# Kernel optimization log

Hardware: AMD Instinct MI355X
Metric: run time of the kernel (lower is better)

The kernel has to match this reference:

```python
import jax, jax.numpy as jnp
import numpy as np

N = 50000       # nodes
E = 500000      # edges (before self loops)
IN = 256        # in_dim
HID = 128       # hidden
HEADS = 2       # GATv2 heads (concat=False -> head mean)
G = 64          # num graphs in batch
SLOPE = 0.2     # leaky_relu negative slope (PyG default)


def setup_inputs() -> dict:
    key = jax.random.key(0)
    ks = jax.random.split(key, 30)
    w = lambda k, shape: jax.random.normal(k, shape, jnp.float32) * 0.05
    inp = {
        "x": jax.random.normal(ks[0], (N, IN), jnp.float32),
        "edge_index": jax.random.randint(ks[1], (2, E), 0, N, dtype=jnp.int64),
        "batch": jnp.sort(jax.random.randint(ks[2], (N,), 0, G, dtype=jnp.int64)),
        # encoder MLP
        "enc_w1": w(ks[3], (HID, IN)),  "enc_b1": w(ks[4], (HID,)),
        "enc_w2": w(ks[5], (HID, HID)), "enc_b2": w(ks[6], (HID,)),
        # GATv2 conv1: lin_l, lin_r -> heads*out; att [H, C]; final bias [C]
        "c1_wl": w(ks[7], (HEADS * HID, HID)),  "c1_bl": w(ks[8], (HEADS * HID,)),
        "c1_wr": w(ks[9], (HEADS * HID, HID)),  "c1_br": w(ks[10], (HEADS * HID,)),
        "c1_att": w(ks[11], (HEADS, HID)),       "c1_bias": w(ks[12], (HID,)),
        # GATv2 conv2
        "c2_wl": w(ks[13], (HEADS * HID, HID)), "c2_bl": w(ks[14], (HEADS * HID,)),
        "c2_wr": w(ks[15], (HEADS * HID, HID)), "c2_br": w(ks[16], (HEADS * HID,)),
        "c2_att": w(ks[17], (HEADS, HID)),       "c2_bias": w(ks[18], (HID,)),
        # attentional pooling gate MLP
        "gate_w1": w(ks[19], (HID, HID)), "gate_b1": w(ks[20], (HID,)),
        "gate_w2": w(ks[21], (1, HID)),   "gate_b2": w(ks[22], (1,)),
        # head MLP
        "head_w1": w(ks[23], (HID, HID)), "head_b1": w(ks[24], (HID,)),
        "head_w2": w(ks[25], (2, HID)),   "head_b2": w(ks[26], (2,)),
    }
    return inp


def _gatv2(x, src, dst, wl, bl, wr, br, att, bias):
    """PyG GATv2Conv, heads=HEADS, concat=False (mean over heads)."""
    n = x.shape[0]
    xl = (x @ wl.T + bl).reshape(n, HEADS, HID)   # source transform
    xr = (x @ wr.T + br).reshape(n, HEADS, HID)   # target transform
    s = jax.nn.leaky_relu(xl[src] + xr[dst], SLOPE)          # [E,H,C]
    e = jnp.einsum('ehc,hc->eh', s, att)                      # [E,H]
    m = jax.ops.segment_max(e, dst, num_segments=n)
    a = jnp.exp(e - m[dst])
    a = a / (jax.ops.segment_sum(a, dst, num_segments=n)[dst] + 1e-16)
    out = jax.ops.segment_sum(a[:, :, None] * xl[src], dst, num_segments=n)
    return out.mean(axis=1) + bias                            # [N,C]


def _forward(x, edge_index, batch,
             enc_w1, enc_b1, enc_w2, enc_b2,
             c1_wl, c1_bl, c1_wr, c1_br, c1_att, c1_bias,
             c2_wl, c2_bl, c2_wr, c2_br, c2_att, c2_bias,
             gate_w1, gate_b1, gate_w2, gate_b2,
             head_w1, head_b1, head_w2, head_b2):
    n = x.shape[0]
    # add self loops (PyG GATv2Conv default add_self_loops=True)
    loop = jnp.arange(n, dtype=edge_index.dtype)
    src = jnp.concatenate([edge_index[0], loop])
    dst = jnp.concatenate([edge_index[1], loop])

    h = jax.nn.relu(x @ enc_w1.T + enc_b1)
    h = jax.nn.relu(h @ enc_w2.T + enc_b2)
    h = jax.nn.relu(_gatv2(h, src, dst, c1_wl, c1_bl, c1_wr, c1_br, c1_att, c1_bias))
    h = jax.nn.relu(_gatv2(h, src, dst, c2_wl, c2_bl, c2_wr, c2_br, c2_att, c2_bias))

    # attentional aggregation: segment-softmax gate over graphs
    gate = (jax.nn.relu(h @ gate_w1.T + gate_b1) @ gate_w2.T + gate_b2)[:, 0]  # [N]
    gm = jax.ops.segment_max(gate, batch, num_segments=G)
    ga = jnp.exp(gate - gm[batch])
    ga = ga / (jax.ops.segment_sum(ga, batch, num_segments=G)[batch] + 1e-16)
    g = jax.ops.segment_sum(ga[:, None] * h, batch, num_segments=G)  # [G,HID]

    out = jax.nn.relu(g @ head_w1.T + head_b1) @ head_w2.T + head_b2  # [G,2]
    # F.normalize(dim=1), eps=1e-12
    norm = jnp.linalg.norm(out, axis=1, keepdims=True)
    return out / jnp.maximum(norm, 1e-12)


def reference(x, edge_index, batch,
              enc_w1, enc_b1, enc_w2, enc_b2,
              c1_wl, c1_bl, c1_wr, c1_br, c1_att, c1_bias,
              c2_wl, c2_bl, c2_wr, c2_br, c2_att, c2_bias,
              gate_w1, gate_b1, gate_w2, gate_b2,
              head_w1, head_b1, head_w2, head_b2):
    return _forward(x, edge_index, batch,
                    enc_w1, enc_b1, enc_w2, enc_b2,
                    c1_wl, c1_bl, c1_wr, c1_br, c1_att, c1_bias,
                    c2_wl, c2_bl, c2_wr, c2_br, c2_att, c2_bias,
                    gate_w1, gate_b1, gate_w2, gate_b2,
                    head_w1, head_b1, head_w2, head_b2)
```

## Files before the change

### kernel.cpp

```cpp
#include <hip/hip_runtime.h>
#include <math.h>

#define CH 128
#define F2 256
#define NG 64
#define PS 16

typedef __attribute__((ext_vector_type(8))) short short8;
typedef __attribute__((ext_vector_type(4))) float f32x4;

__device__ inline ushort f2bf_t(float x) { return (ushort)(__float_as_uint(x) >> 16); }
__device__ inline ushort f2bf_r(float x) {
  uint u = __float_as_uint(x);
  return (ushort)((u + 0x7fffu + ((u >> 16) & 1u)) >> 16);
}
__device__ inline float bf2f(ushort h) { return __uint_as_float(((uint)h) << 16); }

__device__ inline void split4(const float4 v, ushort4& h, ushort4& l) {
  h.x = f2bf_t(v.x); l.x = f2bf_t(v.x - bf2f(h.x));
  h.y = f2bf_t(v.y); l.y = f2bf_t(v.y - bf2f(h.y));
  h.z = f2bf_t(v.z); l.z = f2bf_t(v.z - bf2f(h.z));
  h.w = f2bf_t(v.w); l.w = f2bf_t(v.w - bf2f(h.w));
}

template<int NT, int ACT, int AF32, int GATE>
__global__ __launch_bounds__(NT * 128) void gemm_full(
    const void* __restrict__ Av, const float* __restrict__ W,
    const float* __restrict__ bias, ushort* __restrict__ Cb,
    const float* __restrict__ w2, const float* __restrict__ b2,
    float* __restrict__ gate, int M, int K) {
  constexpr int Nn = NT * 64;
  constexpr int NTH = NT * 128;
  constexpr int AC4 = AF32 ? (1024 / NTH) : 1;
  constexpr int AC2 = AF32 ? 1 : (512 / NTH);
  __shared__ ushort Ab[128 * 40];
  __shared__ ushort Wh[Nn * 40], Wl[Nn * 40];
  const int tid = threadIdx.x;
  const int lane = tid & 63, wid = tid >> 6;
  const int wm = wid / NT, wn = wid % NT;
  const int bm = blockIdx.x * 128;
  const int fr = lane & 15, fg = lane >> 4;
  const float* Af = (const float*)Av;
  const ushort* Ah16 = (const ushort*)Av;

  f32x4 acc[4][4];
#pragma unroll
  for (int i = 0; i < 4; ++i)
#pragma unroll
    for (int j = 0; j < 4; ++j) acc[i][j] = (f32x4)0.f;

  float4 avf[AC4];
  short8 avb[AC2];
  float4 wv[4];
  auto load_tiles = [&](int k0) {
    if constexpr (AF32) {
#pragma unroll
      for (int i2 = 0; i2 < AC4; ++i2) {
        const int c = tid + NTH * i2;
        const int row = c >> 3, kq = (c & 7) * 4;
        const int gr = bm + row;
        avf[i2] = (gr < M) ? *(const float4*)(Af + (size_t)gr * K + k0 + kq)
                           : make_float4(0.f, 0.f, 0.f, 0.f);
      }
    } else {
#pragma unroll
      for (int i2 = 0; i2 < AC2; ++i2) {
        const int c = tid + NTH * i2;
        const int row = c >> 2, kq = (c & 3) * 8;
        const int gr = bm + row;
        avb[i2] = (gr < M) ? *(const short8*)(Ah16 + (size_t)gr * K + k0 + kq)
                           : (short8)0;
      }
    }
#pragma unroll
    for (int i2 = 0; i2 < 4; ++i2) {
      const int c = tid + NTH * i2;
      const int row = c >> 3, kq = (c & 7) * 4;
      wv[i2] = *(const float4*)(W + (size_t)row * K + k0 + kq);
    }
  };

  load_tiles(0);
  for (int k0 = 0; k0 < K; k0 += 32) {
    __syncthreads();
    if constexpr (AF32) {
#pragma unroll
      for (int i2 = 0; i2 < AC4; ++i2) {
        const int c = tid + NTH * i2;
        const int row = c >> 3, kq = (c & 7) * 4;
        const float4 v = avf[i2];
        ushort4 h;
        h.x = f2bf_r(v.x); h.y = f2bf_r(v.y); h.z = f2bf_r(v.z); h.w = f2bf_r(v.w);
        *(ushort4*)&Ab[row * 40 + kq] = h;
      }
    } else {
#pragma unroll
      for (int i2 = 0; i2 < AC2; ++i2) {
        const int c = tid + NTH * i2;
        const int row = c >> 2, kq = (c & 3) * 8;
        *(short8*)&Ab[row * 40 + kq] = avb[i2];
      }
    }
#pragma unroll
    for (int i2 = 0; i2 < 4; ++i2) {
      const int c = tid + NTH * i2;
      const int row = c >> 3, kq = (c & 7) * 4;
      ushort4 h, l; split4(wv[i2], h, l);
      *(ushort4*)&Wh[row * 40 + kq] = h;
      *(ushort4*)&Wl[row * 40 + kq] = l;
    }
    __syncthreads();
    if (k0 + 32 < K) load_tiles(k0 + 32);
    short8 fa[4];
#pragma unroll
    for (int i = 0; i < 4; ++i)
      fa[i] = *(const short8*)&Ab[(wm * 64 + i * 16 + fr) * 40 + fg * 8];
#pragma unroll
    for (int j = 0; j < 4; ++j) {
      const int wbase = (wn * 64 + j * 16 + fr) * 40 + fg * 8;
      const short8 fwh = *(const short8*)&Wh[wbase];
      const short8 fwl = *(const short8*)&Wl[wbase];
#pragma unroll
      for (int i = 0; i < 4; ++i) {
        acc[i][j] = __builtin_amdgcn_mfma_f32_16x16x32_bf16(fa[i], fwh, acc[i][j], 0, 0, 0);
        acc[i][j] = __builtin_amdgcn_mfma_f32_16x16x32_bf16(fa[i], fwl, acc[i][j], 0, 0, 0);
      }
    }
  }
  if constexpr (GATE) {
    __shared__ float gpart[2][128];
    const float b2v = b2[0];
    float rsum[4][4];
#pragma unroll
    for (int i = 0; i < 4; ++i)
#pragma unroll
      for (int r = 0; r < 4; ++r) rsum[i][r] = 0.f;
#pragma unroll
    for (int j = 0; j < 4; ++j) {
      const int col = wn * 64 + j * 16 + fr;
      const float bv = bias[col], wv2 = w2[col];
#pragma unroll
      for (int i = 0; i < 4; ++i)
#pragma unroll
        for (int r = 0; r < 4; ++r) {
          const float v = fmaxf(acc[i][j][r] + bv, 0.f);
          rsum[i][r] += v * wv2;
        }
    }
#pragma unroll
    for (int i = 0; i < 4; ++i)
#pragma unroll
      for (int r = 0; r < 4; ++r) {
        float v = rsum[i][r];
        v += __shfl_xor(v, 1);
        v += __shfl_xor(v, 2);
        v += __shfl_xor(v, 4);
        v += __shfl_xor(v, 8);
        rsum[i][r] = v;
      }
    if (fr == 0) {
#pragma unroll
      for (int i = 0; i < 4; ++i)
#pragma unroll
        for (int r = 0; r < 4; ++r)
          gpart[wn][wm * 64 + i * 16 + fg * 4 + r] = rsum[i][r];
    }
    __syncthreads();
    if (tid < 128) {
      const int row = bm + tid;
      if (row < M) gate[row] = gpart[0][tid] + gpart[1][tid] + b2v;
    }
  } else {
#pragma unroll
    for (int j = 0; j < 4; ++j) {
      const int col = wn * 64 + j * 16 + fr;
      const float bv = bias[col];
#pragma unroll
      for (int i = 0; i < 4; ++i)
#pragma unroll
        for (int r = 0; r < 4; ++r) {
          const int row = bm + wm * 64 + i * 16 + fg * 4 + r;
          if (row < M) {
            float v = acc[i][j][r] + bv;
            if (ACT) v = fmaxf(v, 0.f);
            Cb[(size_t)row * Nn + col] = f2bf_r(v);
          }
        }
    }
  }
}

__global__ void fill_zero_i32(int* __restrict__ p, int n) {
  int i = blockIdx.x * blockDim.x + threadIdx.x;
  if (i < n) p[i] = 0;
}
__global__ void edge_hist(const int* __restrict__ ei, int E, int Etot, int* __restrict__ counts) {
  int e = blockIdx.x * blockDim.x + threadIdx.x;
  if (e >= Etot) return;
  int d = (e < E) ? ei[E + e] : (e - E);
  atomicAdd(&counts[d], 1);
}
__global__ __launch_bounds__(1024) void hist_sums(const int* __restrict__ counts,
                                                  int* __restrict__ bsum, int n) {
  __shared__ int sm[1024];
  const int tid = threadIdx.x;
  const int idx = blockIdx.x * 1024 + tid;
  sm[tid] = (idx < n) ? counts[idx] : 0;
  __syncthreads();
  for (int off = 512; off; off >>= 1) {
    if (tid < off) sm[tid] += sm[tid + off];
    __syncthreads();
  }
  if (tid == 0) bsum[blockIdx.x] = sm[0];
}
__global__ void scan_bsums(const int* __restrict__ bsum, int* __restrict__ boff, int nb) {
  if (threadIdx.x == 0 && blockIdx.x == 0) {
    int run = 0;
    for (int i = 0; i < nb; ++i) { boff[i] = run; run += bsum[i]; }
  }
}
__global__ __launch_bounds__(1024) void scan_apply(const int* __restrict__ counts,
                                                   const int* __restrict__ boff,
                                                   int* __restrict__ indptr,
                                                   int* __restrict__ cur, int n) {
  __shared__ int sm[1024];
  const int tid = threadIdx.x;
  const int idx = blockIdx.x * 1024 + tid;
  const int v = (idx < n) ? counts[idx] : 0;
  sm[tid] = v;
  __syncthreads();
  for (int off = 1; off < 1024; off <<= 1) {
    const int t = (tid >= off) ? sm[tid - off] : 0;
    __syncthreads();
    sm[tid] += t;
    __syncthreads();
  }
  const int excl = boff[blockIdx.x] + sm[tid] - v;
  if (idx < n) {
    indptr[idx] = excl;
    cur[idx] = excl;
    if (idx == n - 1) indptr[n] = excl + v;
  }
}
__global__ void edge_scatter(const int* __restrict__ ei, int E, int Etot,
                             int* __restrict__ cur, int* __restrict__ csr_src) {
  int e = blockIdx.x * blockDim.x + threadIdx.x;
  if (e >= Etot) return;
  int s, d;
  if (e < E) { s = ei[e]; d = ei[E + e]; } else { s = e - E; d = s; }
  int p = atomicAdd(&cur[d], 1);
  csr_src[p] = s;
}

__global__ __launch_bounds__(256) void fused_conv(
    const int* __restrict__ indptr, const int* __restrict__ csr_src,
    const ushort* __restrict__ XLb, const ushort* __restrict__ XRb,
    const float* __restrict__ att, const float* __restrict__ bias,
    ushort* __restrict__ OUT, int N) {
  int node = (int)((blockIdx.x * (size_t)256 + threadIdx.x) >> 6);
  if (node >= N) return;
  const int lane = threadIdx.x & 63;
  const int f = lane * 4;
  const ushort4 xrb = *(const ushort4*)(XRb + (size_t)node * F2 + f);
  const float xr0 = bf2f(xrb.x), xr1 = bf2f(xrb.y), xr2 = bf2f(xrb.z), xr3 = bf2f(xrb.w);
  const float4 at = *(const float4*)(att + f);
  const int s = indptr[node], e = indptr[node + 1];
  float m = -3.4e38f, dsum = 0.f;
  float a0 = 0.f, a1 = 0.f, a2 = 0.f, a3 = 0.f;

  auto score = [&](float x0, float x1, float x2, float x3) -> float {
    float v0 = x0 + xr0; v0 = v0 > 0.f ? v0 : 0.2f * v0;
    float v1 = x1 + xr1; v1 = v1 > 0.f ? v1 : 0.2f * v1;
    float v2 = x2 + xr2; v2 = v2 > 0.f ? v2 : 0.2f * v2;
    float v3 = x3 + xr3; v3 = v3 > 0.f ? v3 : 0.2f * v3;
    return v0 * at.x + v1 * at.y + v2 * at.z + v3 * at.w;
  };
  auto update = [&](float p, float x0, float x1, float x2, float x3) {
    if (__all(p <= m)) {
      const float w = __expf(p - m);
      dsum += w;
      a0 += w * x0; a1 += w * x1; a2 += w * x2; a3 += w * x3;
    } else {
      const float mn = fmaxf(m, p);
      const float sc = __expf(m - mn);
      const float w  = __expf(p - mn);
      dsum = dsum * sc + w;
      a0 = a0 * sc + w * x0; a1 = a1 * sc + w * x1;
      a2 = a2 * sc + w * x2; a3 = a3 * sc + w * x3;
      m = mn;
    }
  };

  int k = s;
  for (; k + 4 <= e; k += 4) {
    const int sn0 = csr_src[k + 0];
    const int sn1 = csr_src[k + 1];
    const int sn2 = csr_src[k + 2];
    const int sn3 = csr_src[k + 3];
    const ushort4 b0 = *(const ushort4*)(XLb + (size_t)sn0 * F2 + f);
    const ushort4 b1 = *(const ushort4*)(XLb + (size_t)sn1 * F2 + f);
    const ushort4 b2 = *(const ushort4*)(XLb + (size_t)sn2 * F2 + f);
    const ushort4 b3 = *(const ushort4*)(XLb + (size_t)sn3 * F2 + f);
    const float x00 = bf2f(b0.x), x01 = bf2f(b0.y), x02 = bf2f(b0.z), x03 = bf2f(b0.w);
    const float x10 = bf2f(b1.x), x11 = bf2f(b1.y), x12 = bf2f(b1.z), x13 = bf2f(b1.w);
    const float x20 = bf2f(b2.x), x21 = bf2f(b2.y), x22 = bf2f(b2.z), x23 = bf2f(b2.w);
    const float x30 = bf2f(b3.x), x31 = bf2f(b3.y), x32 = bf2f(b3.z), x33 = bf2f(b3.w);
    float p0 = score(x00, x01, x02, x03);
    float p1 = score(x10, x11, x12, x13);
    float p2 = score(x20, x21, x22, x23);
    float p3 = score(x30, x31, x32, x33);
#pragma unroll
    for (int d2 = 1; d2 <= 16; d2 <<= 1) {
      p0 += __shfl_xor(p0, d2);
      p1 += __shfl_xor(p1, d2);
      p2 += __shfl_xor(p2, d2);
      p3 += __shfl_xor(p3, d2);
    }
    update(p0, x00, x01, x02, x03);
    update(p1, x10, x11, x12, x13);
    update(p2, x20, x21, x22, x23);
    update(p3, x30, x31, x32, x33);
  }
  for (; k < e; ++k) {
    const int sn = csr_src[k];
    const ushort4 xb = *(const ushort4*)(XLb + (size_t)sn * F2 + f);
    const float x0 = bf2f(xb.x), x1 = bf2f(xb.y), x2 = bf2f(xb.z), x3 = bf2f(xb.w);
    float p = score(x0, x1, x2, x3);
#pragma unroll
    for (int d2 = 1; d2 <= 16; d2 <<= 1) p += __shfl_xor(p, d2);
    update(p, x0, x1, x2, x3);
  }

  const float inv = 1.f / (dsum + 1e-16f);
  a0 *= inv; a1 *= inv; a2 *= inv; a3 *= inv;
  float o0 = 0.5f * (a0 + __shfl_xor(a0, 32));
  float o1 = 0.5f * (a1 + __shfl_xor(a1, 32));
  float o2 = 0.5f * (a2 + __shfl_xor(a2, 32));
  float o3 = 0.5f * (a3 + __shfl_xor(a3, 32));
  if (lane < 32) {
    ushort4 r;
    r.x = f2bf_r(fmaxf(o0 + bias[f + 0], 0.f));
    r.y = f2bf_r(fmaxf(o1 + bias[f + 1], 0.f));
    r.z = f2bf_r(fmaxf(o2 + bias[f + 2], 0.f));
    r.w = f2bf_r(fmaxf(o3 + bias[f + 3], 0.f));
    *(ushort4*)(OUT + (size_t)node * CH + f) = r;
  }
}

__global__ __launch_bounds__(256) void pool_stats(
    const float* __restrict__ gate, const int* __restrict__ batch,
    float* __restrict__ pm, float* __restrict__ pd, int N) {
  const int g = blockIdx.x, tid = threadIdx.x;
  int lo = 0, hi = N;
  while (lo < hi) { int mid = (lo + hi) >> 1; if (batch[mid] < g) lo = mid + 1; else hi = mid; }
  const int s = lo;
  lo = 0; hi = N;
  while (lo < hi) { int mid = (lo + hi) >> 1; if (batch[mid] < g + 1) lo = mid + 1; else hi = mid; }
  const int e = lo;
  __shared__ float red[256];
  float m = -3.4e38f;
  for (int n = s + tid; n < e; n += 256) m = fmaxf(m, gate[n]);
  red[tid] = m; __syncthreads();
  for (int off = 128; off; off >>= 1) {
    if (tid < off) red[tid] = fmaxf(red[tid], red[tid + off]);
    __syncthreads();
  }
  m = red[0]; __syncthreads();
  float d = 0.f;
  for (int n = s + tid; n < e; n += 256) d += expf(gate[n] - m);
  red[tid] = d; __syncthreads();
  for (int off = 128; off; off >>= 1) {
    if (tid < off) red[tid] += red[tid + off];
    __syncthreads();
  }
  if (tid == 0) { pm[g] = m; pd[g] = red[0]; }
}

__global__ __launch_bounds__(128) void pool_partial(
    const float* __restrict__ gate, const int* __restrict__ batch,
    const float* __restrict__ pm, const float* __restrict__ pd,
    const ushort* __restrict__ H, float* __restrict__ PART, int N) {
  const int g = blockIdx.x / PS, j = blockIdx.x % PS;
  const int tid = threadIdx.x;
  int lo = 0, hi = N;
  while (lo < hi) { int mid = (lo + hi) >> 1; if (batch[mid] < g) lo = mid + 1; else hi = mid; }
  const int s = lo;
  lo = 0; hi = N;
  while (lo < hi) { int mid = (lo + hi) >> 1; if (batch[mid] < g + 1) lo = mid + 1; else hi = mid; }
  const int e = lo;
  const int len = e - s;
  const int per = (len + PS - 1) / PS;
  const int ns = s + j * per;
  const int ne = min(ns + per, e);
  const float m = pm[g];
  const float inv = 1.f / (pd[g] + 1e-16f);
  float acc = 0.f;
  for (int n = ns; n < ne; ++n) {
    const float w = expf(gate[n] - m);
    acc += w * bf2f(H[(size_t)n * CH + tid]);
  }
  PART[(size_t)blockIdx.x * CH + tid] = acc * inv;
}
__global__ __launch_bounds__(128) void pool_reduce(
    const float* __restrict__ PART, float* __restrict__ Gout) {
  const int g = blockIdx.x, tid = threadIdx.x;
  float acc = 0.f;
#pragma unroll
  for (int j = 0; j < PS; ++j) acc += PART[(size_t)(g * PS + j) * CH + tid];
  Gout[(size_t)g * CH + tid] = acc;
}

__global__ __launch_bounds__(128) void head_kernel(
    const float* __restrict__ Gin, const float* __restrict__ w1, const float* __restrict__ b1,
    const float* __restrict__ w2, const float* __restrict__ b2, float* __restrict__ out) {
  const int g = blockIdx.x, tid = threadIdx.x;
  __shared__ float gs[128], ts[128], o[2];
  gs[tid] = Gin[(size_t)g * CH + tid];
  __syncthreads();
  float a = b1[tid];
  for (int k = 0; k < CH; ++k) a += w1[tid * CH + k] * gs[k];
  ts[tid] = fmaxf(a, 0.f);
  __syncthreads();
  if (tid < 2) {
    float v = b2[tid];
    for (int d2 = 0; d2 < CH; ++d2) v += w2[tid * CH + d2] * ts[d2];
    o[tid] = v;
  }
  __syncthreads();
  if (tid == 0) {
    float nrm = sqrtf(o[0] * o[0] + o[1] * o[1]);
    nrm = fmaxf(nrm, 1e-12f);
    out[g * 2 + 0] = o[0] / nrm;
    out[g * 2 + 1] = o[1] / nrm;
  }
}

extern "C" void kernel_launch(void* const* d_in, const int* in_sizes, int n_in,
                              void* d_out, int out_size, void* d_ws, size_t ws_size,
                              hipStream_t stream) {
  const float* x       = (const float*)d_in[0];
  const int*   ei      = (const int*)d_in[1];
  const int*   batch   = (const int*)d_in[2];
  const float* enc_w1  = (const float*)d_in[3];
  const float* enc_b1  = (const float*)d_in[4];
  const float* enc_w2  = (const float*)d_in[5];
  const float* enc_b2  = (const float*)d_in[6];
  const float* c1_wl   = (const float*)d_in[7];
  const float* c1_bl   = (const float*)d_in[8];
  const float* c1_wr   = (const float*)d_in[9];
  const float* c1_br   = (const float*)d_in[10];
  const float* c1_att  = (const float*)d_in[11];
  const float* c1_bias = (const float*)d_in[12];
  const float* c2_wl   = (const float*)d_in[13];
  const float* c2_bl   = (const float*)d_in[14];
  const float* c2_wr   = (const float*)d_in[15];
  const float* c2_br   = (const float*)d_in[16];
  const float* c2_att  = (const float*)d_in[17];
  const float* c2_bias = (const float*)d_in[18];
  const float* gate_w1 = (const float*)d_in[19];
  const float* gate_b1 = (const float*)d_in[20];
  const float* gate_w2 = (const float*)d_in[21];
  const float* gate_b2 = (const float*)d_in[22];
  const float* head_w1 = (const float*)d_in[23];
  const float* head_b1 = (const float*)d_in[24];
  const float* head_w2 = (const float*)d_in[25];
  const float* head_b2 = (const float*)d_in[26];

  const int N    = in_sizes[2];
  const int E    = in_sizes[1] / 2;
  const int INF_ = in_sizes[0] / N;
  const int Etot = E + N;
  const int NBLK = (N + 1023) / 1024;

  char* wp = (char*)d_ws;
  auto alloc = [&](size_t bytes) -> void* {
    void* p = (void*)wp;
    wp += (bytes + 255) & ~(size_t)255;
    return p;
  };
  ushort* XLb    = (ushort*)alloc((size_t)N * F2 * 2);
  ushort* XRb    = (ushort*)alloc((size_t)N * F2 * 2);
  ushort* Ha     = (ushort*)alloc((size_t)N * CH * 2);
  ushort* Hb     = (ushort*)alloc((size_t)N * CH * 2);
  ushort* Hc     = (ushort*)alloc((size_t)N * CH * 2);
  int*    counts = (int*)alloc((size_t)N * 4);
  int*    indptr = (int*)alloc((size_t)(N + 1) * 4);
  int*    cur    = (int*)alloc((size_t)N * 4);
  int*    csr_src= (int*)alloc((size_t)Etot * 4);
  int*    bsum   = (int*)alloc((size_t)NBLK * 4);
  int*    boff   = (int*)alloc((size_t)NBLK * 4);
  float*  gateb  = (float*)alloc((size_t)N * 4);
  float*  GS     = (float*)alloc((size_t)NG * CH * 4);
  float*  pm     = (float*)alloc((size_t)NG * 4);
  float*  pd     = (float*)alloc((size_t)NG * 4);
  float*  PART   = (float*)alloc((size_t)NG * PS * CH * 4);

  const dim3 blk(256);
  const int gM = (N + 127) / 128;

  gemm_full<2,1,1,0><<<gM, 256, 0, stream>>>(x, enc_w1, enc_b1, Ha,
                                             nullptr, nullptr, nullptr, N, INF_);
  gemm_full<2,1,0,0><<<gM, 256, 0, stream>>>(Ha, enc_w2, enc_b2, Hb,
                                             nullptr, nullptr, nullptr, N, CH);

  fill_zero_i32<<<(N + 255) / 256, blk, 0, stream>>>(counts, N);
  edge_hist<<<(Etot + 255) / 256, blk, 0, stream>>>(ei, E, Etot, counts);
  hist_sums<<<NBLK, 1024, 0, stream>>>(counts, bsum, N);
  scan_bsums<<<1, 64, 0, stream>>>(bsum, boff, NBLK);
  scan_apply<<<NBLK, 1024, 0, stream>>>(counts, boff, indptr, cur, N);
  edge_scatter<<<(Etot + 255) / 256, blk, 0, stream>>>(ei, E, Etot, cur, csr_src);

  gemm_full<4,0,0,0><<<gM, 512, 0, stream>>>(Hb, c1_wl, c1_bl, XLb,
                                             nullptr, nullptr, nullptr, N, CH);
  gemm_full<4,0,0,0><<<gM, 512, 0, stream>>>(Hb, c1_wr, c1_br, XRb,
                                             nullptr, nullptr, nullptr, N, CH);
  fused_conv<<<(N + 3) / 4, blk, 0, stream>>>(indptr, csr_src, XLb, XRb, c1_att, c1_bias, Hc, N);

  gemm_full<4,0,0,0><<<gM, 512, 0, stream>>>(Hc, c2_wl, c2_bl, XLb,
                                             nullptr, nullptr, nullptr, N, CH);
  gemm_full<4,0,0,0><<<gM, 512, 0, stream>>>(Hc, c2_wr, c2_br, XRb,
                                             nullptr, nullptr, nullptr, N, CH);
  fused_conv<<<(N + 3) / 4, blk, 0, stream>>>(indptr, csr_src, XLb, XRb, c2_att, c2_bias, Hb, N);

  gemm_full<2,1,0,1><<<gM, 256, 0, stream>>>(Hb, gate_w1, gate_b1, nullptr,
                                             gate_w2, gate_b2, gateb, N, CH);

  pool_stats<<<NG, blk, 0, stream>>>(gateb, batch, pm, pd, N);
  pool_partial<<<NG * PS, 128, 0, stream>>>(gateb, batch, pm, pd, Hb, PART, N);
  pool_reduce<<<NG, 128, 0, stream>>>(PART, GS);

  head_kernel<<<NG, 128, 0, stream>>>(GS, head_w1, head_b1, head_w2, head_b2, (float*)d_out);
}
```

Before: 535.2 us.

## Pre-split weights to bf16 once, fuse lin_l/lin_r GEMMs, drop lo-term for conv weights

Adds a single kernel that converts all weight matrices to bf16 hi/lo pairs up front, so the GEMM blocks no longer re-split fp32 weights every K step. The lin_l and lin_r projections of each GATv2 conv now run as one 1024-thread GEMM that writes to two outputs, which removes a launch and reads the A tile once. For the conv weights only a single rounded bf16 copy is kept, which halves MFMA work there but lowers precision compared with the previous hi+lo compensated product. LDS is now dynamically sized.

```diff
diff --git a/kernel.cpp b/kernel.cpp
--- a/kernel.cpp
+++ b/kernel.cpp
@@ -16,32 +16,42 @@
 }
 __device__ inline float bf2f(ushort h) { return __uint_as_float(((uint)h) << 16); }
 
-__device__ inline void split4(const float4 v, ushort4& h, ushort4& l) {
-  h.x = f2bf_t(v.x); l.x = f2bf_t(v.x - bf2f(h.x));
-  h.y = f2bf_t(v.y); l.y = f2bf_t(v.y - bf2f(h.y));
-  h.z = f2bf_t(v.z); l.z = f2bf_t(v.z - bf2f(h.z));
-  h.w = f2bf_t(v.w); l.w = f2bf_t(v.w - bf2f(h.w));
-}
-
-template<int NT, int ACT, int AF32, int GATE>
+struct WSpec { const float* src; ushort* hi; ushort* lo; int n; };
+struct WPack { WSpec w[7]; };
+__global__ __launch_bounds__(256) void split_weights(WPack p) {
+  const WSpec s = p.w[blockIdx.y];
+  for (int i = blockIdx.x * 256 + threadIdx.x; i < s.n; i += gridDim.x * 256) {
+    const float v = s.src[i];
+    if (s.lo) {
+      const ushort h = f2bf_t(v);
+      s.hi[i] = h;
+      s.lo[i] = f2bf_t(v - bf2f(h));
+    } else {
+      s.hi[i] = f2bf_r(v);
+    }
+  }
+}
+
+template<int NT, int ACT, int AF32, int GATE, int SPLIT, int WSPLIT>
 __global__ __launch_bounds__(NT * 128) void gemm_full(
-    const void* __restrict__ Av, const float* __restrict__ W,
-    const float* __restrict__ bias, ushort* __restrict__ Cb,
-    const float* __restrict__ w2, const float* __restrict__ b2,
-    float* __restrict__ gate, int M, int K) {
+    const void* __restrict__ Av, const ushort* __restrict__ Whi,
+    const ushort* __restrict__ Wlo, const float* __restrict__ bias,
+    const float* __restrict__ bias2, ushort* __restrict__ Cb0,
+    ushort* __restrict__ Cb1, const float* __restrict__ w2,
+    const float* __restrict__ b2, float* __restrict__ gate, int M, int K) {
   constexpr int Nn = NT * 64;
   constexpr int NTH = NT * 128;
-  constexpr int AC4 = AF32 ? (1024 / NTH) : 1;
-  constexpr int AC2 = AF32 ? 1 : (512 / NTH);
-  __shared__ ushort Ab[128 * 40];
-  __shared__ ushort Wh[Nn * 40], Wl[Nn * 40];
+  constexpr int ACF = AF32 ? (1024 / NTH) : 1;
+  constexpr int ACB = AF32 ? 1 : ((512 + NTH - 1) / NTH);
+  extern __shared__ ushort smem[];
+  ushort* Ab = smem;
+  ushort* Wh = smem + 128 * 40;
+  ushort* Wl = WSPLIT ? (Wh + Nn * 40) : Wh;
   const int tid = threadIdx.x;
   const int lane = tid & 63, wid = tid >> 6;
   const int wm = wid / NT, wn = wid % NT;
   const int bm = blockIdx.x * 128;
   const int fr = lane & 15, fg = lane >> 4;
-  const float* Af = (const float*)Av;
-  const ushort* Ah16 = (const ushort*)Av;
 
   f32x4 acc[4][4];
 #pragma unroll
@@ -49,34 +59,38 @@
 #pragma unroll
     for (int j = 0; j < 4; ++j) acc[i][j] = (f32x4)0.f;
 
-  float4 avf[AC4];
-  short8 avb[AC2];
-  float4 wv[4];
+  float4 avf[ACF];
+  short8 avb[ACB];
+  short8 wvh[2], wvl[2];
   auto load_tiles = [&](int k0) {
     if constexpr (AF32) {
 #pragma unroll
-      for (int i2 = 0; i2 < AC4; ++i2) {
+      for (int i2 = 0; i2 < ACF; ++i2) {
         const int c = tid + NTH * i2;
         const int row = c >> 3, kq = (c & 7) * 4;
         const int gr = bm + row;
-        avf[i2] = (gr < M) ? *(const float4*)(Af + (size_t)gr * K + k0 + kq)
+        avf[i2] = (gr < M) ? *(const float4*)((const float*)Av + (size_t)gr * K + k0 + kq)
                            : make_float4(0.f, 0.f, 0.f, 0.f);
       }
     } else {
 #pragma unroll
-      for (int i2 = 0; i2 < AC2; ++i2) {
+      for (int i2 = 0; i2 < ACB; ++i2) {
         const int c = tid + NTH * i2;
-        const int row = c >> 2, kq = (c & 3) * 8;
-        const int gr = bm + row;
-        avb[i2] = (gr < M) ? *(const short8*)(Ah16 + (size_t)gr * K + k0 + kq)
-                           : (short8)0;
+        if (c < 512) {
+          const int row = c >> 2, kq = (c & 3) * 8;
+          const int gr = bm + row;
+          avb[i2] = (gr < M) ? *(const short8*)((const ushort*)Av + (size_t)gr * K + k0 + kq)
+                             : (short8)0;
+        }
       }
     }
 #pragma unroll
-    for (int i2 = 0; i2 < 4; ++i2) {
+    for (int i2 = 0; i2 < 2; ++i2) {
       const int c = tid + NTH * i2;
-      const int row = c >> 3, kq = (c & 7) * 4;
-      wv[i2] = *(const float4*)(W + (size_t)row * K + k0 + kq);
+      const int row = c >> 2, kq = (c & 3) * 8;
+      wvh[i2] = *(const short8*)(Whi + (size_t)row * K + k0 + kq);
+      if constexpr (WSPLIT)
+        wvl[i2] = *(const short8*)(Wlo + (size_t)row * K + k0 + kq);
     }
   };
 
@@ -85,7 +99,7 @@
     __syncthreads();
     if constexpr (AF32) {
 #pragma unroll
-      for (int i2 = 0; i2 < AC4; ++i2) {
+      for (int i2 = 0; i2 < ACF; ++i2) {
         const int c = tid + NTH * i2;
         const int row = c >> 3, kq = (c & 7) * 4;
         const float4 v = avf[i2];
@@ -95,19 +109,20 @@
       }
     } else {
 #pragma unroll
-      for (int i2 = 0; i2 < AC2; ++i2) {
+      for (int i2 = 0; i2 < ACB; ++i2) {
         const int c = tid + NTH * i2;
-        const int row = c >> 2, kq = (c & 3) * 8;
-        *(short8*)&Ab[row * 40 + kq] = avb[i2];
+        if (c < 512) {
+          const int row = c >> 2, kq = (c & 3) * 8;
+          *(short8*)&Ab[row * 40 + kq] = avb[i2];
+        }
       }
     }
 #pragma unroll
-    for (int i2 = 0; i2 < 4; ++i2) {
+    for (int i2 = 0; i2 < 2; ++i2) {
       const int c = tid + NTH * i2;
-      const int row = c >> 3, kq = (c & 7) * 4;
-      ushort4 h, l; split4(wv[i2], h, l);
-      *(ushort4*)&Wh[row * 40 + kq] = h;
-      *(ushort4*)&Wl[row * 40 + kq] = l;
+      const int row = c >> 2, kq = (c & 3) * 8;
+      *(short8*)&Wh[row * 40 + kq] = wvh[i2];
+      if constexpr (WSPLIT) *(short8*)&Wl[row * 40 + kq] = wvl[i2];
     }
     __syncthreads();
     if (k0 + 32 < K) load_tiles(k0 + 32);
@@ -119,11 +134,14 @@
     for (int j = 0; j < 4; ++j) {
       const int wbase = (wn * 64 + j * 16 + fr) * 40 + fg * 8;
       const short8 fwh = *(const short8*)&Wh[wbase];
-      const short8 fwl = *(const short8*)&Wl[wbase];
-#pragma unroll
-      for (int i = 0; i < 4; ++i) {
+#pragma unroll
+      for (int i = 0; i < 4; ++i)
         acc[i][j] = __builtin_amdgcn_mfma_f32_16x16x32_bf16(fa[i], fwh, acc[i][j], 0, 0, 0);
-        acc[i][j] = __builtin_amdgcn_mfma_f32_16x16x32_bf16(fa[i], fwl, acc[i][j], 0, 0, 0);
+      if constexpr (WSPLIT) {
+        const short8 fwl = *(const short8*)&Wl[wbase];
+#pragma unroll
+        for (int i = 0; i < 4; ++i)
+          acc[i][j] = __builtin_amdgcn_mfma_f32_16x16x32_bf16(fa[i], fwl, acc[i][j], 0, 0, 0);
       }
     }
   }
@@ -174,7 +192,9 @@
 #pragma unroll
     for (int j = 0; j < 4; ++j) {
       const int col = wn * 64 + j * 16 + fr;
-      const float bv = bias[col];
+      float bv;
+      if constexpr (SPLIT) bv = (wn < NT / 2) ? bias[col] : bias2[col - Nn / 2];
+      else                 bv = bias[col];
 #pragma unroll
       for (int i = 0; i < 4; ++i)
 #pragma unroll
@@ -183,7 +203,13 @@
           if (row < M) {
             float v = acc[i][j][r] + bv;
             if (ACT) v = fmaxf(v, 0.f);
-            Cb[(size_t)row * Nn + col] = f2bf_r(v);
+            const ushort o = f2bf_r(v);
+            if constexpr (SPLIT) {
+              if (wn < NT / 2) Cb0[(size_t)row * (Nn / 2) + col] = o;
+              else             Cb1[(size_t)row * (Nn / 2) + col - Nn / 2] = o;
+            } else {
+              Cb0[(size_t)row * Nn + col] = o;
+            }
           }
         }
     }
@@ -494,14 +520,31 @@
   float*  pm     = (float*)alloc((size_t)NG * 4);
   float*  pd     = (float*)alloc((size_t)NG * 4);
   float*  PART   = (float*)alloc((size_t)NG * PS * CH * 4);
+  ushort* We1h = (ushort*)alloc((size_t)CH * INF_ * 2);
+  ushort* We1l = (ushort*)alloc((size_t)CH * INF_ * 2);
+  ushort* We2h = (ushort*)alloc((size_t)CH * CH * 2);
+  ushort* We2l = (ushort*)alloc((size_t)CH * CH * 2);
+  ushort* Wc1  = (ushort*)alloc((size_t)2 * F2 * CH * 2);
+  ushort* Wc2  = (ushort*)alloc((size_t)2 * F2 * CH * 2);
+  ushort* Wgh  = (ushort*)alloc((size_t)CH * CH * 2);
+  ushort* Wgl  = (ushort*)alloc((size_t)CH * CH * 2);
 
   const dim3 blk(256);
   const int gM = (N + 127) / 128;
-
-  gemm_full<2,1,1,0><<<gM, 256, 0, stream>>>(x, enc_w1, enc_b1, Ha,
-                                             nullptr, nullptr, nullptr, N, INF_);
-  gemm_full<2,1,0,0><<<gM, 256, 0, stream>>>(Ha, enc_w2, enc_b2, Hb,
-                                             nullptr, nullptr, nullptr, N, CH);
+  const int nw = F2 * CH;
+
+  WPack wpk;
+  wpk.w[0] = { enc_w1,  We1h,       We1l,    CH * INF_ };
+  wpk.w[1] = { enc_w2,  We2h,       We2l,    CH * CH };
+  wpk.w[2] = { c1_wl,   Wc1,        nullptr, nw };
+  wpk.w[3] = { c1_wr,   Wc1 + nw,   nullptr, nw };
+  wpk.w[4] = { c2_wl,   Wc2,        nullptr, nw };
+  wpk.w[5] = { c2_wr,   Wc2 + nw,   nullptr, nw };
+  wpk.w[6] = { gate_w1, Wgh,        Wgl,     CH * CH };
+  split_weights<<<dim3(128, 7), blk, 0, stream>>>(wpk);
+
+  const int LDS2 = (128 * 40 + 2 * 128 * 40) * 2;
+  const int LDS8 = (128 * 40 + 512 * 40) * 2;
 
   fill_zero_i32<<<(N + 255) / 256, blk, 0, stream>>>(counts, N);
   edge_hist<<<(Etot + 255) / 256, blk, 0, stream>>>(ei, E, Etot, counts);
@@ -510,20 +553,21 @@
   scan_apply<<<NBLK, 1024, 0, stream>>>(counts, boff, indptr, cur, N);
   edge_scatter<<<(Etot + 255) / 256, blk, 0, stream>>>(ei, E, Etot, cur, csr_src);
 
-  gemm_full<4,0,0,0><<<gM, 512, 0, stream>>>(Hb, c1_wl, c1_bl, XLb,
-                                             nullptr, nullptr, nullptr, N, CH);
-  gemm_full<4,0,0,0><<<gM, 512, 0, stream>>>(Hb, c1_wr, c1_br, XRb,
-                                             nullptr, nullptr, nullptr, N, CH);
+  gemm_full<2,1,1,0,0,1><<<gM, 256, LDS2, stream>>>(
+      x, We1h, We1l, enc_b1, nullptr, Ha, nullptr, nullptr, nullptr, nullptr, N, INF_);
+  gemm_full<2,1,0,0,0,1><<<gM, 256, LDS2, stream>>>(
+      Ha, We2h, We2l, enc_b2, nullptr, Hb, nullptr, nullptr, nullptr, nullptr, N, CH);
+
+  gemm_full<8,0,0,0,1,0><<<gM, 1024, LDS8, stream>>>(
+      Hb, Wc1, nullptr, c1_bl, c1_br, XLb, XRb, nullptr, nullptr, nullptr, N, CH);
   fused_conv<<<(N + 3) / 4, blk, 0, stream>>>(indptr, csr_src, XLb, XRb, c1_att, c1_bias, Hc, N);
 
-  gemm_full<4,0,0,0><<<gM, 512, 0, stream>>>(Hc, c2_wl, c2_bl, XLb,
-                                             nullptr, nullptr, nullptr, N, CH);
-  gemm_full<4,0,0,0><<<gM, 512, 0, stream>>>(Hc, c2_wr, c2_br, XRb,
-                                             nullptr, nullptr, nullptr, N, CH);
+  gemm_full<8,0,0,0,1,0><<<gM, 1024, LDS8, stream>>>(
+      Hc, Wc2, nullptr, c2_bl, c2_br, XLb, XRb, nullptr, nullptr, nullptr, N, CH);
   fused_conv<<<(N + 3) / 4, blk, 0, stream>>>(indptr, csr_src, XLb, XRb, c2_att, c2_bias, Hb, N);
 
-  gemm_full<2,1,0,1><<<gM, 256, 0, stream>>>(Hb, gate_w1, gate_b1, nullptr,
-                                             gate_w2, gate_b2, gateb, N, CH);
+  gemm_full<2,1,0,1,0,1><<<gM, 256, LDS2, stream>>>(
+      Hb, Wgh, Wgl, gate_b1, nullptr, nullptr, nullptr, gate_w2, gate_b2, gateb, N, CH);
 
   pool_stats<<<NG, blk, 0, stream>>>(gateb, batch, pm, pd, N);
   pool_partial<<<NG * PS, 128, 0, stream>>>(gateb, batch, pm, pd, Hb, PART, N);
```

Result: faster. 489.0 us (-8.6%).
